# Kernel optimization log

Measured on AMD Instinct MI355X. Metric: run time of the kernel, lower is better.

The kernel has to match this reference:

```python
import jax, jax.numpy as jnp
import numpy as np

N_NODES = 100_000
N_EDGES = 1_000_000
D_IN = 128
D_OUT = 64


def setup_inputs() -> dict:
    key = jax.random.key(0)
    k1, k2, k3 = jax.random.split(key, 3)
    x = jax.random.normal(k1, (N_NODES, D_IN), dtype=jnp.float32)
    edge_index = jax.random.randint(k2, (2, N_EDGES), 0, N_NODES)
    W = jax.random.normal(k3, (D_IN, D_OUT), dtype=jnp.float32) / np.float32(np.sqrt(D_IN))
    b = jnp.zeros((D_OUT,), dtype=jnp.float32)
    weight = jnp.float32(0.5)
    temperature = jnp.float32(10.0)
    return {"x": x, "edge_index": edge_index, "weight": weight,
            "temperature": temperature, "W": W, "b": b}


def gcn_conv(x, edge_index, W, b):
    # PyG GCNConv: add self loops, symmetric deg normalization, then aggregate.
    src, dst = edge_index[0], edge_index[1]
    h = x @ W                                                   # [N, D_OUT]
    deg = jnp.ones((N_NODES,), h.dtype).at[dst].add(jnp.ones((src.shape[0],), h.dtype))
    dinv = jax.lax.rsqrt(deg)
    norm = dinv[src] * dinv[dst]                                # [E]
    agg = jax.ops.segment_sum(h[src] * norm[:, None], dst, num_segments=N_NODES)
    # self-loop contribution: norm = deg^-1/2 * deg^-1/2 = 1/deg
    return agg + h * (1.0 / deg)[:, None] + b


def entropy_fn(h, edge_index, temperature):
    # Boltzmann entropy of per-node Dirichlet energies.
    src, dst = edge_index[0], edge_index[1]
    e = jax.ops.segment_sum(jnp.sum((h[dst] - h[src]) ** 2, axis=1),
                            dst, num_segments=N_NODES)          # [N]
    logp = jax.nn.log_softmax(-e / temperature)
    return -jnp.sum(jnp.exp(logp) * logp)


def reference(x, edge_index, weight, temperature, W, b):
    h = gcn_conv(x, edge_index, W, b)
    g = jax.grad(entropy_fn)(h, edge_index, temperature)
    g = g * temperature  # scale_by_temperature=True
    return h + weight * g
```

## Files before the change

### kernel.cpp

```cpp
#include <hip/hip_runtime.h>

#define DIN  128
#define DOUT 64
#define TN   64
#define XP   132
#define BW   512
#define BSH  9
#define EPC  4096
#define NSTATB 400

__global__ __launch_bounds__(256) void k_countboth(const int* __restrict__ src,
                                                   const int* __restrict__ dst,
                                                   unsigned* __restrict__ counts,
                                                   int NBUK, int NC, int E) {
    __shared__ int h0[256], h1[256];
    for (int j = threadIdx.x; j < NBUK; j += 256) { h0[j] = 0; h1[j] = 0; }
    __syncthreads();
    int start = blockIdx.x * EPC;
    int end = min(start + EPC, E);
    for (int i = start + threadIdx.x; i < end; i += 256) {
        atomicAdd(&h0[dst[i] >> BSH], 1);
        atomicAdd(&h1[src[i] >> BSH], 1);
    }
    __syncthreads();
    int M = NBUK * NC;
    for (int j = threadIdx.x; j < NBUK; j += 256) {
        counts[j * NC + blockIdx.x]     = (unsigned)h0[j];
        counts[M + j * NC + blockIdx.x] = (unsigned)h1[j];
    }
}

__global__ __launch_bounds__(256) void k_scanA(const unsigned* __restrict__ data,
                                               unsigned* __restrict__ bsums, int n) {
    __shared__ unsigned s[256];
    int i = blockIdx.x * 256 + threadIdx.x;
    s[threadIdx.x] = (i < n) ? data[i] : 0u;
    __syncthreads();
    for (int st = 128; st > 0; st >>= 1) {
        if (threadIdx.x < st) s[threadIdx.x] += s[threadIdx.x + st];
        __syncthreads();
    }
    if (threadIdx.x == 0) bsums[blockIdx.x] = s[0];
}

__global__ __launch_bounds__(1024) void k_scan2(unsigned* __restrict__ bsums, int NB) {
    __shared__ unsigned s[1024];
    int tid = threadIdx.x;
    unsigned v = (tid < NB) ? bsums[tid] : 0u;
    s[tid] = v;
    __syncthreads();
    for (int st = 1; st < 1024; st <<= 1) {
        unsigned t = (tid >= st) ? s[tid - st] : 0u;
        __syncthreads();
        s[tid] += t;
        __syncthreads();
    }
    if (tid < NB) bsums[tid] = s[tid] - v;
}

__global__ __launch_bounds__(256) void k_scanC(unsigned* __restrict__ data,
                                               const unsigned* __restrict__ bsums, int n) {
    __shared__ unsigned s[256];
    int i = blockIdx.x * 256 + threadIdx.x;
    unsigned v = (i < n) ? data[i] : 0u;
    s[threadIdx.x] = v;
    __syncthreads();
    for (int st = 1; st < 256; st <<= 1) {
        unsigned t = (threadIdx.x >= st) ? s[threadIdx.x - st] : 0u;
        __syncthreads();
        s[threadIdx.x] += t;
        __syncthreads();
    }
    if (i < n) data[i] = s[threadIdx.x] - v + bsums[blockIdx.x];
}

__global__ __launch_bounds__(256) void k_bucket(const int* __restrict__ key,
                                                const int* __restrict__ other,
                                                const unsigned* __restrict__ counts,
                                                int dirOff, unsigned dirBase,
                                                int2* __restrict__ bucketed,
                                                int NBUK, int NC, int E) {
    __shared__ int cur[256];
    for (int j = threadIdx.x; j < NBUK; j += 256)
        cur[j] = (int)(counts[dirOff + j * NC + blockIdx.x] - dirBase);
    __syncthreads();
    int start = blockIdx.x * EPC;
    int end = min(start + EPC, E);
    for (int i = start + threadIdx.x; i < end; i += 256) {
        int k = key[i], o = other[i];
        int pos = atomicAdd(&cur[k >> BSH], 1);
        bucketed[pos] = make_int2(k, o);
    }
}

__global__ __launch_bounds__(256) void k_csr(const int2* __restrict__ bucketed,
                                             const unsigned* __restrict__ counts,
                                             unsigned* __restrict__ off,
                                             int* __restrict__ pay,
                                             unsigned* __restrict__ cnt,
                                             float* __restrict__ dinv,
                                             int dirOff, unsigned dirBase,
                                             int NBUK, int NC, int N, int E) {
    __shared__ int sH[BW];
    __shared__ int sS[2][BW];
    __shared__ int sC[BW];
    int b = blockIdx.x;
    int base = (int)(counts[dirOff + b * NC] - dirBase);
    int end  = (b + 1 < NBUK) ? (int)(counts[dirOff + (b + 1) * NC] - dirBase) : E;

    for (int j = threadIdx.x; j < BW; j += 256) sH[j] = 0;
    __syncthreads();
    for (int i = base + threadIdx.x; i < end; i += 256)
        atomicAdd(&sH[bucketed[i].x & (BW - 1)], 1);
    __syncthreads();
    for (int j = threadIdx.x; j < BW; j += 256) sS[0][j] = sH[j];
    __syncthreads();
    int pin = 0;
    for (int st = 1; st < BW; st <<= 1) {
        for (int j = threadIdx.x; j < BW; j += 256) {
            int v = sS[pin][j];
            if (j >= st) v += sS[pin][j - st];
            sS[pin ^ 1][j] = v;
        }
        __syncthreads();
        pin ^= 1;
    }
    int lo = b * BW;
    for (int j = threadIdx.x; j < BW; j += 256) {
        int excl = j ? sS[pin][j - 1] : 0;
        sC[j] = excl;
        int n = lo + j;
        if (n < N) {
            off[n] = (unsigned)(base + excl);
            if (cnt) {
                cnt[n] = (unsigned)sH[j];
                dinv[n] = rsqrtf((float)sH[j] + 1.f);
            }
        }
    }
    if (threadIdx.x == 0 && b == NBUK - 1) off[N] = (unsigned)E;
    __syncthreads();
    for (int i = base + threadIdx.x; i < end; i += 256) {
        int2 p = bucketed[i];
        int pos = base + atomicAdd(&sC[p.x & (BW - 1)], 1);
        pay[pos] = p.y;
    }
}

__global__ __launch_bounds__(256) void k_gemm(const float* __restrict__ x,
                                              const float* __restrict__ W,
                                              const float* __restrict__ dinv,
                                              float* __restrict__ h0s, int N) {
    __shared__ float Xs[TN * XP];
    __shared__ float Ws[DIN * DOUT];

    for (int i = threadIdx.x; i < DIN * DOUT / 4; i += 256)
        ((float4*)Ws)[i] = ((const float4*)W)[i];

    int base = blockIdx.x * TN;
    int kq = threadIdx.x & 31;
    int rr = threadIdx.x >> 5;
#pragma unroll
    for (int it = 0; it < 8; ++it) {
        int r = rr + it * 8;
        int n = base + r;
        float4 v = make_float4(0.f, 0.f, 0.f, 0.f);
        if (n < N) v = ((const float4*)(x + (size_t)n * DIN))[kq];
        *((float4*)(Xs + r * XP + 4 * kq)) = v;
    }
    __syncthreads();

    int tx = threadIdx.x & 15;
    int ty = threadIdx.x >> 4;
    float acc[4][4] = {};

#pragma unroll 4
    for (int k = 0; k < DIN; k += 4) {
        float4 a0 = *((float4*)(Xs + (4 * ty + 0) * XP + k));
        float4 a1 = *((float4*)(Xs + (4 * ty + 1) * XP + k));
        float4 a2 = *((float4*)(Xs + (4 * ty + 2) * XP + k));
        float4 a3 = *((float4*)(Xs + (4 * ty + 3) * XP + k));
        float4 w0 = *((float4*)(Ws + (k + 0) * DOUT + 4 * tx));
        float4 w1 = *((float4*)(Ws + (k + 1) * DOUT + 4 * tx));
        float4 w2 = *((float4*)(Ws + (k + 2) * DOUT + 4 * tx));
        float4 w3 = *((float4*)(Ws + (k + 3) * DOUT + 4 * tx));
#define ROW(j, aj)                                                             \
        acc[j][0] = fmaf(aj.x, w0.x, fmaf(aj.y, w1.x, fmaf(aj.z, w2.x, fmaf(aj.w, w3.x, acc[j][0])))); \
        acc[j][1] = fmaf(aj.x, w0.y, fmaf(aj.y, w1.y, fmaf(aj.z, w2.y, fmaf(aj.w, w3.y, acc[j][1])))); \
        acc[j][2] = fmaf(aj.x, w0.z, fmaf(aj.y, w1.z, fmaf(aj.z, w2.z, fmaf(aj.w, w3.z, acc[j][2])))); \
        acc[j][3] = fmaf(aj.x, w0.w, fmaf(aj.y, w1.w, fmaf(aj.z, w2.w, fmaf(aj.w, w3.w, acc[j][3]))));
        ROW(0, a0) ROW(1, a1) ROW(2, a2) ROW(3, a3)
#undef ROW
    }

#pragma unroll
    for (int j = 0; j < 4; ++j) {
        int n = base + 4 * ty + j;
        if (n < N) {
            float dv = dinv[n];
            float4 o = make_float4(acc[j][0] * dv, acc[j][1] * dv,
                                   acc[j][2] * dv, acc[j][3] * dv);
            *((float4*)(h0s + (size_t)n * DOUT + 4 * tx)) = o;
        }
    }
}

__global__ __launch_bounds__(256) void k_agg(const unsigned* __restrict__ off,
                                             const int* __restrict__ pay,
                                             const float* __restrict__ dinv,
                                             const float* __restrict__ h0s,
                                             const float* __restrict__ b,
                                             float* __restrict__ h, int N) {
    int t = threadIdx.x;
    int grp = t >> 4;
    int q = t & 15;
    int n = blockIdx.x * 16 + grp;
    if (n >= N) return;
    unsigned beg = off[n], end = off[n + 1];
    float4 acc = make_float4(0.f, 0.f, 0.f, 0.f);
    for (unsigned base2 = beg; base2 < end; base2 += 16) {
        unsigned idx = base2 + q;
        int pd = (idx < end) ? pay[idx] : 0;
        int jmax = (int)min(16u, end - base2);
        int j = 0;
        for (; j + 4 <= jmax; j += 4) {
            int s0 = __shfl(pd, j + 0, 16);
            int s1 = __shfl(pd, j + 1, 16);
            int s2 = __shfl(pd, j + 2, 16);
            int s3 = __shfl(pd, j + 3, 16);
            float4 a0 = *(const float4*)(h0s + (size_t)s0 * DOUT + 4 * q);
            float4 a1 = *(const float4*)(h0s + (size_t)s1 * DOUT + 4 * q);
            float4 a2 = *(const float4*)(h0s + (size_t)s2 * DOUT + 4 * q);
            float4 a3 = *(const float4*)(h0s + (size_t)s3 * DOUT + 4 * q);
            acc.x += (a0.x + a1.x) + (a2.x + a3.x);
            acc.y += (a0.y + a1.y) + (a2.y + a3.y);
            acc.z += (a0.z + a1.z) + (a2.z + a3.z);
            acc.w += (a0.w + a1.w) + (a2.w + a3.w);
        }
        for (; j < jmax; ++j) {
            int s = __shfl(pd, j, 16);
            float4 a = *(const float4*)(h0s + (size_t)s * DOUT + 4 * q);
            acc.x += a.x; acc.y += a.y; acc.z += a.z; acc.w += a.w;
        }
    }
    float dv = dinv[n];
    float4 hs = *(const float4*)(h0s + (size_t)n * DOUT + 4 * q);
    float4 bv = *(const float4*)(b + 4 * q);
    float4 o;
    o.x = dv * (acc.x + hs.x) + bv.x;
    o.y = dv * (acc.y + hs.y) + bv.y;
    o.z = dv * (acc.z + hs.z) + bv.z;
    o.w = dv * (acc.w + hs.w) + bv.w;
    *(float4*)(h + (size_t)n * DOUT + 4 * q) = o;
}

__global__ __launch_bounds__(256) void k_energy(const unsigned* __restrict__ off,
                                                const int* __restrict__ pay,
                                                const float* __restrict__ h,
                                                float* __restrict__ e,
                                                float* __restrict__ S, int N) {
    int t = threadIdx.x;
    int grp = t >> 4;
    int q = t & 15;
    int n = blockIdx.x * 16 + grp;
    if (n >= N) return;
    unsigned beg = off[n], end = off[n + 1];
    float4 hm = *(const float4*)(h + (size_t)n * DOUT + 4 * q);
    float4 Sa = make_float4(0.f, 0.f, 0.f, 0.f);
    float esum = 0.f;
    for (unsigned base2 = beg; base2 < end; base2 += 16) {
        unsigned idx = base2 + q;
        int pd = (idx < end) ? pay[idx] : 0;
        int jmax = (int)min(16u, end - base2);
        int j = 0;
        for (; j + 4 <= jmax; j += 4) {
            int s0 = __shfl(pd, j + 0, 16);
            int s1 = __shfl(pd, j + 1, 16);
            int s2 = __shfl(pd, j + 2, 16);
            int s3 = __shfl(pd, j + 3, 16);
            float4 a0 = *(const float4*)(h + (size_t)s0 * DOUT + 4 * q);
            float4 a1 = *(const float4*)(h + (size_t)s1 * DOUT + 4 * q);
            float4 a2 = *(const float4*)(h + (size_t)s2 * DOUT + 4 * q);
            float4 a3 = *(const float4*)(h + (size_t)s3 * DOUT + 4 * q);
            Sa.x += (a0.x + a1.x) + (a2.x + a3.x);
            Sa.y += (a0.y + a1.y) + (a2.y + a3.y);
            Sa.z += (a0.z + a1.z) + (a2.z + a3.z);
            Sa.w += (a0.w + a1.w) + (a2.w + a3.w);
            float dx, dy, dz, dw;
            dx = hm.x - a0.x; dy = hm.y - a0.y; dz = hm.z - a0.z; dw = hm.w - a0.w;
            esum += dx * dx + dy * dy + dz * dz + dw * dw;
            dx = hm.x - a1.x; dy = hm.y - a1.y; dz = hm.z - a1.z; dw = hm.w - a1.w;
            esum += dx * dx + dy * dy + dz * dz + dw * dw;
            dx = hm.x - a2.x; dy = hm.y - a2.y; dz = hm.z - a2.z; dw = hm.w - a2.w;
            esum += dx * dx + dy * dy + dz * dz + dw * dw;
            dx = hm.x - a3.x; dy = hm.y - a3.y; dz = hm.z - a3.z; dw = hm.w - a3.w;
            esum += dx * dx + dy * dy + dz * dz + dw * dw;
        }
        for (; j < jmax; ++j) {
            int s = __shfl(pd, j, 16);
            float4 a = *(const float4*)(h + (size_t)s * DOUT + 4 * q);
            Sa.x += a.x; Sa.y += a.y; Sa.z += a.z; Sa.w += a.w;
            float dx = hm.x - a.x, dy = hm.y - a.y, dz = hm.z - a.z, dw = hm.w - a.w;
            esum += dx * dx + dy * dy + dz * dz + dw * dw;
        }
    }
#pragma unroll
    for (int m = 1; m <= 8; m <<= 1) esum += __shfl_xor(esum, m, 16);
    if (q == 0) e[n] = esum;
    *(float4*)(S + (size_t)n * DOUT + 4 * q) = Sa;
}

__global__ __launch_bounds__(256) void k_stats1(const float* __restrict__ e,
                                                const float* __restrict__ Tptr,
                                                float* __restrict__ part, int N) {
    float T = *Tptr;
    float m = -3.4e38f;
    int i0 = blockIdx.x * 256 + threadIdx.x;
    int stride = gridDim.x * 256;
    for (int i = i0; i < N; i += stride) m = fmaxf(m, -e[i] / T);
    __shared__ float sm[256];
    sm[threadIdx.x] = m;
    __syncthreads();
    for (int s = 128; s > 0; s >>= 1) {
        if (threadIdx.x < s) sm[threadIdx.x] = fmaxf(sm[threadIdx.x], sm[threadIdx.x + s]);
        __syncthreads();
    }
    float bm = sm[0];
    __syncthreads();
    float z = 0.f, mm = 0.f;
    for (int i = i0; i < N; i += stride) {
        float t = -e[i] / T - bm;
        float w = __expf(t);
        z += w;
        mm += w * t;
    }
    __shared__ float sz[256], sM[256];
    sz[threadIdx.x] = z;
    sM[threadIdx.x] = mm;
    __syncthreads();
    for (int s = 128; s > 0; s >>= 1) {
        if (threadIdx.x < s) {
            sz[threadIdx.x] += sz[threadIdx.x + s];
            sM[threadIdx.x] += sM[threadIdx.x + s];
        }
        __syncthreads();
    }
    if (threadIdx.x == 0) {
        part[blockIdx.x * 3 + 0] = bm;
        part[blockIdx.x * 3 + 1] = sz[0];
        part[blockIdx.x * 3 + 2] = sM[0];
    }
}

__global__ __launch_bounds__(256) void k_stats2(const float* __restrict__ part,
                                                float* __restrict__ st, int P) {
    __shared__ float sm[256];
    float m = -3.4e38f;
    for (int i = threadIdx.x; i < P; i += 256) m = fmaxf(m, part[3 * i]);
    sm[threadIdx.x] = m;
    __syncthreads();
    for (int s = 128; s > 0; s >>= 1) {
        if (threadIdx.x < s) sm[threadIdx.x] = fmaxf(sm[threadIdx.x], sm[threadIdx.x + s]);
        __syncthreads();
    }
    float gm = sm[0];
    __syncthreads();
    float Z = 0.f, M = 0.f;
    for (int i = threadIdx.x; i < P; i += 256) {
        float mb = part[3 * i], zb = part[3 * i + 1], Mb = part[3 * i + 2];
        float d = mb - gm, eb = __expf(d);
        Z += eb * zb;
        M += eb * (Mb + d * zb);
    }
    __shared__ float sz[256], sM2[256];
    sz[threadIdx.x] = Z;
    sM2[threadIdx.x] = M;
    __syncthreads();
    for (int s = 128; s > 0; s >>= 1) {
        if (threadIdx.x < s) {
            sz[threadIdx.x] += sz[threadIdx.x + s];
            sM2[threadIdx.x] += sM2[threadIdx.x + s];
        }
        __syncthreads();
    }
    if (threadIdx.x == 0) {
        st[0] = gm;
        st[1] = sz[0];
        st[2] = sM2[0];
    }
}

__global__ __launch_bounds__(256) void k_coef(const float* __restrict__ e,
                                              const float* __restrict__ Tptr,
                                              const float* __restrict__ st,
                                              float* __restrict__ c, int N) {
    int n = blockIdx.x * 256 + threadIdx.x;
    if (n >= N) return;
    float T = *Tptr;
    float gm = st[0], Z = st[1], M = st[2];
    float logZ = logf(Z);
    float H = logZ - M / Z;
    float t = -e[n] / T - gm;
    float lp = t - logZ;
    c[n] = expf(lp) * (lp + H);
}

__global__ __launch_bounds__(256) void k_grad_final(const unsigned* __restrict__ off,
                                                    const int* __restrict__ pay,
                                                    const float* __restrict__ c,
                                                    const float* __restrict__ h,
                                                    const float* __restrict__ S,
                                                    const unsigned* __restrict__ cnt,
                                                    const float* __restrict__ wptr,
                                                    float* __restrict__ out, int N) {
    int t = threadIdx.x;
    int grp = t >> 4;
    int q = t & 15;
    int n = blockIdx.x * 16 + grp;
    if (n >= N) return;
    unsigned beg = off[n], end = off[n + 1];
    float A = 0.f;
    float4 B = make_float4(0.f, 0.f, 0.f, 0.f);
    for (unsigned base2 = beg; base2 < end; base2 += 16) {
        unsigned idx = base2 + q;
        int pd = 0;
        float cv = 0.f;
        if (idx < end) {
            pd = pay[idx];
            cv = c[pd];
        }
        int jmax = (int)min(16u, end - base2);
        int j = 0;
        for (; j + 4 <= jmax; j += 4) {
            int s0 = __shfl(pd, j + 0, 16);
            int s1 = __shfl(pd, j + 1, 16);
            int s2 = __shfl(pd, j + 2, 16);
            int s3 = __shfl(pd, j + 3, 16);
            float c0 = __shfl(cv, j + 0, 16);
            float c1 = __shfl(cv, j + 1, 16);
            float c2 = __shfl(cv, j + 2, 16);
            float c3 = __shfl(cv, j + 3, 16);
            float4 a0 = *(const float4*)(h + (size_t)s0 * DOUT + 4 * q);
            float4 a1 = *(const float4*)(h + (size_t)s1 * DOUT + 4 * q);
            float4 a2 = *(const float4*)(h + (size_t)s2 * DOUT + 4 * q);
            float4 a3 = *(const float4*)(h + (size_t)s3 * DOUT + 4 * q);
            A += (c0 + c1) + (c2 + c3);
            B.x = fmaf(c0, a0.x, fmaf(c1, a1.x, fmaf(c2, a2.x, fmaf(c3, a3.x, B.x))));
            B.y = fmaf(c0, a0.y, fmaf(c1, a1.y, fmaf(c2, a2.y, fmaf(c3, a3.y, B.y))));
            B.z = fmaf(c0, a0.z, fmaf(c1, a1.z, fmaf(c2, a2.z, fmaf(c3, a3.z, B.z))));
            B.w = fmaf(c0, a0.w, fmaf(c1, a1.w, fmaf(c2, a2.w, fmaf(c3, a3.w, B.w))));
        }
        for (; j < jmax; ++j) {
            int s = __shfl(pd, j, 16);
            float cj = __shfl(cv, j, 16);
            float4 a = *(const float4*)(h + (size_t)s * DOUT + 4 * q);
            A += cj;
            B.x = fmaf(cj, a.x, B.x);
            B.y = fmaf(cj, a.y, B.y);
            B.z = fmaf(cj, a.z, B.z);
            B.w = fmaf(cj, a.w, B.w);
        }
    }
    size_t idx4 = (size_t)n * DOUT + 4 * q;
    float4 hm = *(const float4*)(h + idx4);
    float4 Sv = *(const float4*)(S + idx4);
    float cn = c[n];
    float cc = (float)cnt[n];
    float w = *wptr;
    float4 o;
    o.x = hm.x + w * (2.f * cn * (cc * hm.x - Sv.x) + 2.f * (A * hm.x - B.x));
    o.y = hm.y + w * (2.f * cn * (cc * hm.y - Sv.y) + 2.f * (A * hm.y - B.y));
    o.z = hm.z + w * (2.f * cn * (cc * hm.z - Sv.z) + 2.f * (A * hm.z - B.z));
    o.w = hm.w + w * (2.f * cn * (cc * hm.w - Sv.w) + 2.f * (A * hm.w - B.w));
    *(float4*)(out + idx4) = o;
}

extern "C" void kernel_launch(void* const* d_in, const int* in_sizes, int n_in,
                              void* d_out, int out_size, void* d_ws, size_t ws_size,
                              hipStream_t stream) {
    const float* x    = (const float*)d_in[0];
    const int*   ei   = (const int*)d_in[1];
    const float* wptr = (const float*)d_in[2];
    const float* Tptr = (const float*)d_in[3];
    const float* W    = (const float*)d_in[4];
    const float* b    = (const float*)d_in[5];
    float* out = (float*)d_out;

    const int N  = in_sizes[0] / DIN;
    const int E  = in_sizes[1] / 2;
    const int NE = N * DOUT;
    const int* src = ei;
    const int* dst = ei + E;

    const int NBUK = (N + BW - 1) / BW;
    const int NC   = (E + EPC - 1) / EPC;
    const int M    = NBUK * NC;
    const int M2   = 2 * M;
    const int NBs  = (M2 + 255) / 256;

    float*    h0s  = (float*)d_ws;
    float*    h    = h0s + NE;
    int2*     bkt  = (int2*)(h + NE);
    int*      pay1 = (int*)(bkt + E);
    int*      pay2 = pay1 + E;
    unsigned* counts = (unsigned*)(pay2 + E);
    unsigned* bsum = counts + M2;
    unsigned* off1 = bsum + 1024;
    unsigned* off2 = off1 + N + 1;
    unsigned* cnt  = off2 + N + 1;
    float*    e    = (float*)(cnt + N);
    float*    c    = e + N;
    float*    dinv = c + N;
    float*    part = dinv + N;
    float*    st   = part + 3 * NSTATB;
    float*    S    = h0s;

    const int nodeG = (N + 15) / 16;
    const int nodeBlocks = (N + 255) / 256;

    k_countboth<<<NC, 256, 0, stream>>>(src, dst, counts, NBUK, NC, E);
    k_scanA<<<NBs, 256, 0, stream>>>(counts, bsum, M2);
    k_scan2<<<1, 1024, 0, stream>>>(bsum, NBs);
    k_scanC<<<NBs, 256, 0, stream>>>(counts, bsum, M2);

    k_bucket<<<NC, 256, 0, stream>>>(dst, src, counts, 0, 0u, bkt, NBUK, NC, E);
    k_csr<<<NBUK, 256, 0, stream>>>(bkt, counts, off1, pay1, cnt, dinv,
                                    0, 0u, NBUK, NC, N, E);
    k_bucket<<<NC, 256, 0, stream>>>(src, dst, counts, M, (unsigned)E, bkt, NBUK, NC, E);
    k_csr<<<NBUK, 256, 0, stream>>>(bkt, counts, off2, pay2, nullptr, nullptr,
                                    M, (unsigned)E, NBUK, NC, N, E);

    k_gemm<<<(N + TN - 1) / TN, 256, 0, stream>>>(x, W, dinv, h0s, N);
    k_agg<<<nodeG, 256, 0, stream>>>(off1, pay1, dinv, h0s, b, h, N);
    k_energy<<<nodeG, 256, 0, stream>>>(off1, pay1, h, e, S, N);
    k_stats1<<<NSTATB, 256, 0, stream>>>(e, Tptr, part, N);
    k_stats2<<<1, 256, 0, stream>>>(part, st, NSTATB);
    k_coef<<<nodeBlocks, 256, 0, stream>>>(e, Tptr, st, c, N);
    k_grad_final<<<nodeG, 256, 0, stream>>>(off2, pay2, c, h, S, cnt, wptr, out, N);
}
```

Baseline: 333.9 us.

## Rewrite GEMM as per-wave 16-row tiles with direct global loads, no LDS

The dense x@W kernel no longer stages X and W tiles in shared memory. Each 64-lane wave now computes 16 output rows, one output column per lane. Each lane reads W straight from global memory, and x rows are fetched as wave-uniform float4 broadcasts. This removes the LDS staging, the block barrier and the shared-memory footprint that limited occupancy. In exchange it relies on cache broadcast for the x reads and gives up the register-tile reuse of W across rows.

```diff
diff --git a/kernel.cpp b/kernel.cpp
--- a/kernel.cpp
+++ b/kernel.cpp
@@ -2,8 +2,7 @@
 
 #define DIN  128
 #define DOUT 64
-#define TN   64
-#define XP   132
+#define GR   128
 #define BW   512
 #define BSH  9
 #define EPC  4096
@@ -147,60 +146,53 @@
     }
 }
 
-__global__ __launch_bounds__(256) void k_gemm(const float* __restrict__ x,
+__global__ __launch_bounds__(512) void k_gemm(const float* __restrict__ x,
                                               const float* __restrict__ W,
                                               const float* __restrict__ dinv,
                                               float* __restrict__ h0s, int N) {
-    __shared__ float Xs[TN * XP];
-    __shared__ float Ws[DIN * DOUT];
-
-    for (int i = threadIdx.x; i < DIN * DOUT / 4; i += 256)
-        ((float4*)Ws)[i] = ((const float4*)W)[i];
-
-    int base = blockIdx.x * TN;
-    int kq = threadIdx.x & 31;
-    int rr = threadIdx.x >> 5;
+    int t = threadIdx.x;
+    int c = t & 63;
+    int wv = __builtin_amdgcn_readfirstlane(t >> 6);
+    int base = blockIdx.x * GR + wv * 16;
+    if (base >= N) return;
+    const float* xw = x + (size_t)base * DIN;
+
+    float acc[16] = {};
+    if (base + 16 <= N) {
+        for (int k = 0; k < DIN; k += 4) {
+            float w0 = W[(k + 0) * DOUT + c];
+            float w1 = W[(k + 1) * DOUT + c];
+            float w2 = W[(k + 2) * DOUT + c];
+            float w3 = W[(k + 3) * DOUT + c];
 #pragma unroll
-    for (int it = 0; it < 8; ++it) {
-        int r = rr + it * 8;
-        int n = base + r;
-        float4 v = make_float4(0.f, 0.f, 0.f, 0.f);
-        if (n < N) v = ((const float4*)(x + (size_t)n * DIN))[kq];
-        *((float4*)(Xs + r * XP + 4 * kq)) = v;
-    }
-    __syncthreads();
-
-    int tx = threadIdx.x & 15;
-    int ty = threadIdx.x >> 4;
-    float acc[4][4] = {};
-
-#pragma unroll 4
-    for (int k = 0; k < DIN; k += 4) {
-        float4 a0 = *((float4*)(Xs + (4 * ty + 0) * XP + k));
-        float4 a1 = *((float4*)(Xs + (4 * ty + 1) * XP + k));
-        float4 a2 = *((float4*)(Xs + (4 * ty + 2) * XP + k));
-        float4 a3 = *((float4*)(Xs + (4 * ty + 3) * XP + k));
-        float4 w0 = *((float4*)(Ws + (k + 0) * DOUT + 4 * tx));
-        float4 w1 = *((float4*)(Ws + (k + 1) * DOUT + 4 * tx));
-        float4 w2 = *((float4*)(Ws + (k + 2) * DOUT + 4 * tx));
-        float4 w3 = *((float4*)(Ws + (k + 3) * DOUT + 4 * tx));
-#define ROW(j, aj)                                                             \
-        acc[j][0] = fmaf(aj.x, w0.x, fmaf(aj.y, w1.x, fmaf(aj.z, w2.x, fmaf(aj.w, w3.x, acc[j][0])))); \
-        acc[j][1] = fmaf(aj.x, w0.y, fmaf(aj.y, w1.y, fmaf(aj.z, w2.y, fmaf(aj.w, w3.y, acc[j][1])))); \
-        acc[j][2] = fmaf(aj.x, w0.z, fmaf(aj.y, w1.z, fmaf(aj.z, w2.z, fmaf(aj.w, w3.z, acc[j][2])))); \
-        acc[j][3] = fmaf(aj.x, w0.w, fmaf(aj.y, w1.w, fmaf(aj.z, w2.w, fmaf(aj.w, w3.w, acc[j][3]))));
-        ROW(0, a0) ROW(1, a1) ROW(2, a2) ROW(3, a3)
-#undef ROW
-    }
-
+            for (int i = 0; i < 16; ++i) {
+                float4 a = *(const float4*)(xw + (size_t)i * DIN + k);
+                acc[i] = fmaf(a.x, w0, fmaf(a.y, w1, fmaf(a.z, w2, fmaf(a.w, w3, acc[i]))));
+            }
+        }
 #pragma unroll
-    for (int j = 0; j < 4; ++j) {
-        int n = base + 4 * ty + j;
-        if (n < N) {
-            float dv = dinv[n];
-            float4 o = make_float4(acc[j][0] * dv, acc[j][1] * dv,
-                                   acc[j][2] * dv, acc[j][3] * dv);
-            *((float4*)(h0s + (size_t)n * DOUT + 4 * tx)) = o;
+        for (int i = 0; i < 16; ++i) {
+            int n = base + i;
+            h0s[(size_t)n * DOUT + c] = acc[i] * dinv[n];
+        }
+    } else {
+        for (int k = 0; k < DIN; k += 4) {
+            float w0 = W[(k + 0) * DOUT + c];
+            float w1 = W[(k + 1) * DOUT + c];
+            float w2 = W[(k + 2) * DOUT + c];
+            float w3 = W[(k + 3) * DOUT + c];
+#pragma unroll
+            for (int i = 0; i < 16; ++i) {
+                if (base + i < N) {
+                    float4 a = *(const float4*)(xw + (size_t)i * DIN + k);
+                    acc[i] = fmaf(a.x, w0, fmaf(a.y, w1, fmaf(a.z, w2, fmaf(a.w, w3, acc[i]))));
+                }
+            }
+        }
+#pragma unroll
+        for (int i = 0; i < 16; ++i) {
+            int n = base + i;
+            if (n < N) h0s[(size_t)n * DOUT + c] = acc[i] * dinv[n];
         }
     }
 }
@@ -530,7 +522,7 @@
     k_csr<<<NBUK, 256, 0, stream>>>(bkt, counts, off2, pay2, nullptr, nullptr,
                                     M, (unsigned)E, NBUK, NC, N, E);
 
-    k_gemm<<<(N + TN - 1) / TN, 256, 0, stream>>>(x, W, dinv, h0s, N);
+    k_gemm<<<(N + GR - 1) / GR, 512, 0, stream>>>(x, W, dinv, h0s, N);
     k_agg<<<nodeG, 256, 0, stream>>>(off1, pay1, dinv, h0s, b, h, N);
     k_energy<<<nodeG, 256, 0, stream>>>(off1, pay1, h, e, S, N);
     k_stats1<<<NSTATB, 256, 0, stream>>>(e, Tptr, part, N);
```

Measured after the change: 411.0 us. 23.1% more time.
